# Kernel tuning notes

Measured on AMD Instinct MI355X. Metric: run time of the kernel, lower is better.

The kernel has to match this reference:

```python
import jax, jax.numpy as jnp
import numpy as np

NUM_HEADS = 16
FEAT_DIM = 1024
COORD_DIM = 128
D_FEAT = FEAT_DIM // NUM_HEADS   # 64
D_COORD = COORD_DIM // NUM_HEADS # 8

def setup_inputs() -> dict:
    key = jax.random.key(0)
    ks = jax.random.split(key, 5)
    B, L, S = 2, 2048, 2048
    qf = jax.random.normal(ks[0], (B, L, FEAT_DIM), dtype=jnp.float32)
    kf = jax.random.normal(ks[1], (B, S, FEAT_DIM), dtype=jnp.float32)
    qc = jax.random.normal(ks[2], (B, L, COORD_DIM), dtype=jnp.float32)
    kc = jax.random.normal(ks[3], (B, S, COORD_DIM), dtype=jnp.float32)
    v = jax.random.normal(ks[4], (B, S, FEAT_DIM), dtype=jnp.float32)
    alpha = jnp.ones((NUM_HEADS,), dtype=jnp.float32)
    return {"qf": qf, "kf": kf, "qc": qc, "kc": kc, "v": v, "alpha": alpha}

def _split_heads(x):
    # (B, L, H*D) -> (B, H, L, D)
    B, L, HD = x.shape
    return x.reshape(B, L, NUM_HEADS, HD // NUM_HEADS).transpose(0, 2, 1, 3)

def reference(qf, kf, qc, kc, v, alpha):
    qfh = _split_heads(qf)  # (B,H,L,Df)
    kfh = _split_heads(kf)  # (B,H,S,Df)
    qch = _split_heads(qc)  # (B,H,L,Dc)
    kch = _split_heads(kc)  # (B,H,S,Dc)
    vh = _split_heads(v)    # (B,H,S,Dv)
    # A = softmax(Qf Kf^T / sqrt(Df) + alpha * Qc Kc^T / sqrt(Dc))
    inv_sf = 1.0 / np.sqrt(D_FEAT).astype(np.float32)
    inv_sc = 1.0 / np.sqrt(D_COORD).astype(np.float32)
    scores = (jnp.einsum('bhld,bhsd->bhls', qfh, kfh) * inv_sf
              + alpha[None, :, None, None]
              * jnp.einsum('bhld,bhsd->bhls', qch, kch) * inv_sc)
    attn = jax.nn.softmax(scores, axis=-1)
    out = jnp.einsum('bhls,bhsd->bhld', attn, vh)  # (B,H,L,Dv)
    B, H, L, Dv = out.shape
    return out.transpose(0, 2, 1, 3).reshape(B, L, H * Dv)
```

## Files before the change

### kernel.cpp

```cpp
#include <hip/hip_runtime.h>
#include <hip/hip_bf16.h>

typedef __bf16 bf16_t;
typedef bf16_t bf16x8 __attribute__((ext_vector_type(8)));
typedef float f32x4 __attribute__((ext_vector_type(4)));
typedef float f32x16 __attribute__((ext_vector_type(16)));

#define NHEADS 16
#define DFEAT 64
#define DCOORD 8
#define SEQ 2048
#define KVBLK 64
#define NT (SEQ / KVBLK)
#define QBLK 128
#define KCOLS 80
#define KROWB (KCOLS * 2)
#define KTILEB (KVBLK * KROWB)
#define VSTRB 80
#define VHALFB (DFEAT * VSTRB)
#define VTILEB (2 * VHALFB)

#define KP_BYTES ((size_t)32 * NT * KTILEB)
#define VT_BYTES ((size_t)32 * NT * VTILEB)

union Bf8 { bf16x8 v; __hip_bfloat16 e[8]; };
union U4  { unsigned u[4]; bf16x8 v; };

static __device__ inline unsigned pack2(float a, float b) {
    union { __hip_bfloat16 h[2]; unsigned u; } x;
    x.h[0] = __float2bfloat16(a); x.h[1] = __float2bfloat16(b);
    return x.u;
}

__global__ __launch_bounds__(256)
void pack_kv(const float* __restrict__ kf, const float* __restrict__ kc,
             const float* __restrict__ v,
             char* __restrict__ kp, char* __restrict__ vt)
{
    __shared__ __align__(16) char tile[KTILEB];
    const int bid = blockIdx.x;
    const int tid = threadIdx.x;

    if (bid < 1024) {
        const int blk = bid;
        const int t  = blk & (NT - 1);
        const int bh = blk >> 5;
        const int b = bh >> 4, h = bh & 15;
        #pragma unroll
        for (int it = 0; it < 2; ++it) {
            const int c = tid + it * 256;
            if (c < 320) {
                const int row = c / 5, cc = c - row * 5;
                const int s = t * KVBLK + row;
                float vv[16];
                if (cc < 4) {
                    const float* p = kf + ((long)b * SEQ + s) * (NHEADS * DFEAT) + h * DFEAT + cc * 16;
                    #pragma unroll
                    for (int i = 0; i < 4; ++i) {
                        float4 f = ((const float4*)p)[i];
                        vv[4*i+0]=f.x; vv[4*i+1]=f.y; vv[4*i+2]=f.z; vv[4*i+3]=f.w;
                    }
                } else {
                    const float* p = kc + ((long)b * SEQ + s) * (NHEADS * DCOORD) + h * DCOORD;
                    float4 f0 = ((const float4*)p)[0];
                    float4 f1 = ((const float4*)p)[1];
                    vv[0]=f0.x; vv[1]=f0.y; vv[2]=f0.z; vv[3]=f0.w;
                    vv[4]=f1.x; vv[5]=f1.y; vv[6]=f1.z; vv[7]=f1.w;
                    #pragma unroll
                    for (int i = 8; i < 16; ++i) vv[i] = 0.f;
                }
                Bf8 w0, w1;
                #pragma unroll
                for (int i = 0; i < 8; ++i) {
                    w0.e[i] = __float2bfloat16(vv[i]);
                    w1.e[i] = __float2bfloat16(vv[i + 8]);
                }
                if (cc < 4) {
                    const int key = (row & 7) << 4;
                    const int base = cc * 32;
                    *(bf16x8*)&tile[row * KROWB + ((base)      ^ key)] = w0.v;
                    *(bf16x8*)&tile[row * KROWB + ((base + 16) ^ key)] = w1.v;
                } else {
                    const int key = (row & 1) << 4;
                    *(bf16x8*)&tile[row * KROWB + 128 + ((0)  ^ key)] = w0.v;
                    *(bf16x8*)&tile[row * KROWB + 128 + ((16) ^ key)] = w1.v;
                }
            }
        }
        __syncthreads();
        const bf16x8* ti = (const bf16x8*)tile;
        bf16x8* o = (bf16x8*)(kp + (long)blk * KTILEB);
        #pragma unroll
        for (int j = 0; j < 3; ++j) {
            const int i = tid + 256 * j;
            if (i < 640) o[i] = ti[i];
        }
    } else {
        const int blk = bid - 1024;
        const int t  = blk & (NT - 1);
        const int bh = blk >> 5;
        const int b = bh >> 4, h = bh & 15;
        const int s = tid >> 2, c = tid & 3;
        const int sh = s >> 5, sl = s & 31;
        const int slot = (sl & ~12) | ((sl & 4) << 1) | ((sl & 8) >> 1);
        const float* src = v + ((long)b * SEQ + t * KVBLK + s) * (NHEADS * DFEAT) + h * DFEAT;
        __hip_bfloat16* vtile = (__hip_bfloat16*)tile;
        #pragma unroll
        for (int c4 = 0; c4 < 4; ++c4) {
            float4 f = ((const float4*)src)[c4 * 4 + c];
            float vals[4] = {f.x, f.y, f.z, f.w};
            #pragma unroll
            for (int ii = 0; ii < 4; ++ii) {
                const int dd = c4 * 16 + c * 4 + ii;
                const int byte = sh * VHALFB + dd * VSTRB + slot * 2;
                vtile[byte >> 1] = __float2bfloat16(vals[ii]);
            }
        }
        __syncthreads();
        const bf16x8* ti = (const bf16x8*)tile;
        bf16x8* o = (bf16x8*)(vt + (long)blk * (long)VTILEB);
        #pragma unroll
        for (int j = 0; j < 3; ++j) {
            const int i = tid + 256 * j;
            if (i < 640) o[i] = ti[i];
        }
    }
}

__global__ __launch_bounds__(256, 2)
void stfa_v11(const float* __restrict__ qf, const float* __restrict__ qc,
              const float* __restrict__ alpha,
              const char* __restrict__ kp, const char* __restrict__ vt,
              float* __restrict__ out)
{
    __shared__ __align__(16) char SMEM[2 * KTILEB + 2 * VTILEB];

    const int tid  = threadIdx.x;
    const int wave = tid >> 6;
    const int lane = tid & 63;
    const int lq   = lane & 31;
    const int hi   = lane >> 5;
    const int qp   = wave >> 1;
    const int sh   = wave & 1;

    const int dd    = blockIdx.x;
    const int bh    = dd & 31;
    const int qtile = dd >> 5;
    const int b = bh >> 4, h = bh & 15;

    const float a_h      = alpha[h];
    const float LOG2E    = 1.4426950408889634f;
    const float qf_scale = 0.125f * LOG2E;
    const float qc_scale = a_h * 0.35355339059327373f * LOG2E;

    const char* kp_bh = kp + (long)bh * NT * KTILEB;

    long voff[5];
    #pragma unroll
    for (int j = 0; j < 5; ++j) {
        const int c = wave + 4 * j;
        voff[j] = (c < 10) ? ((long)c * 1024 + lane * 16)
                           : ((long)KP_BYTES + (long)(c - 10) * 1024 + lane * 16);
    }
    int ldsoff[5];
    #pragma unroll
    for (int j = 0; j < 5; ++j) {
        const int c = wave + 4 * j;
        ldsoff[j] = (c < 10) ? c * 1024 : 2 * KTILEB + (c - 10) * 1024;
    }

    auto stage = [&](const char* kg_run, const int BB) {
        #pragma unroll
        for (int j = 0; j < 5; ++j) {
            __builtin_amdgcn_global_load_lds(
                (const __attribute__((address_space(1))) void*)(kg_run + voff[j]),
                (__attribute__((address_space(3))) void*)(SMEM + ldsoff[j] + BB), 16, 0, 0);
        }
    };

    const int krow = sh * 32 + lq;
    int qkaddr[5];
    #pragma unroll
    for (int ks = 0; ks < 5; ++ks) {
        int off;
        if (ks < 4) off = (ks * 32 + hi * 16) ^ ((lq & 7) << 4);
        else        off = 128 + ((hi * 16) ^ ((lq & 1) << 4));
        qkaddr[ks] = krow * KROWB + off;
    }
    int pvaddr[4];
    #pragma unroll
    for (int dt = 0; dt < 2; ++dt)
        #pragma unroll
        for (int ks = 0; ks < 2; ++ks)
            pvaddr[dt * 2 + ks] = sh * VHALFB + (dt * 32 + lq) * VSTRB + ks * 32 + hi * 16;

    const int qrowA = qtile * QBLK + qp * 64 + lq;
    const int qrowB = qrowA + 32;

    bf16x8 qfragA[5], qfragB[5];
    #pragma unroll
    for (int set = 0; set < 2; ++set) {
        const int qrow = set ? qrowB : qrowA;
        const float* qfp = qf + ((long)b * SEQ + qrow) * (NHEADS * DFEAT) + h * DFEAT;
        const float* qcp = qc + ((long)b * SEQ + qrow) * (NHEADS * DCOORD) + h * DCOORD;
        #pragma unroll
        for (int ks = 0; ks < 4; ++ks) {
            const float* p = qfp + ks * 16 + hi * 8;
            float4 f0 = *(const float4*)p;
            float4 f1 = *(const float4*)(p + 4);
            Bf8 q;
        q.e[0] = __float2bfloat16(f0.x * qf_scale); q.e[1] = __float2bfloat16(f0.y * qf_scale);
        q.e[2] = __float2bfloat16(f0.z * qf_scale); q.e[3] = __float2bfloat16(f0.w * qf_scale);
        q.e[4] = __float2bfloat16(f1.x * qf_scale); q.e[5] = __float2bfloat16(f1.y * qf_scale);
        q.e[6] = __float2bfloat16(f1.z * qf_scale); q.e[7] = __float2bfloat16(f1.w * qf_scale);
            if (set) qfragB[ks] = q.v; else qfragA[ks] = q.v;
        }
        Bf8 q;
        #pragma unroll
        for (int i = 0; i < 8; ++i) q.e[i] = __float2bfloat16(0.0f);
        if (hi == 0) {
            float4 c0 = *(const float4*)qcp;
            float4 c1 = *(const float4*)(qcp + 4);
            q.e[0] = __float2bfloat16(c0.x * qc_scale); q.e[1] = __float2bfloat16(c0.y * qc_scale);
            q.e[2] = __float2bfloat16(c0.z * qc_scale); q.e[3] = __float2bfloat16(c0.w * qc_scale);
            q.e[4] = __float2bfloat16(c1.x * qc_scale); q.e[5] = __float2bfloat16(c1.y * qc_scale);
            q.e[6] = __float2bfloat16(c1.z * qc_scale); q.e[7] = __float2bfloat16(c1.w * qc_scale);
        }
        if (set) qfragB[4] = q.v; else qfragA[4] = q.v;
    }

    f32x16 oaccA[2], oaccB[2];
    #pragma unroll
    for (int dt = 0; dt < 2; ++dt)
        #pragma unroll
        for (int r = 0; r < 16; ++r) { oaccA[dt][r] = 0.f; oaccB[dt][r] = 0.f; }
    float lA = 0.f, lB = 0.f;

    auto body = [&](const int KB, const int VB) {
        f32x16 sA, sB;
        #pragma unroll
        for (int r = 0; r < 16; ++r) { sA[r] = 0.f; sB[r] = 0.f; }
        __builtin_amdgcn_s_setprio(1);
        #pragma unroll
        for (int ks = 0; ks < 5; ++ks) {
            bf16x8 kfrag = *(const bf16x8*)&SMEM[KB + qkaddr[ks]];
            sA = __builtin_amdgcn_mfma_f32_32x32x16_bf16(kfrag, qfragA[ks], sA, 0, 0, 0);
            sB = __builtin_amdgcn_mfma_f32_32x32x16_bf16(kfrag, qfragB[ks], sB, 0, 0, 0);
        }
        __builtin_amdgcn_s_setprio(0);

        bf16x8 pA[2], pB[2];
        {
            float p[16];
            #pragma unroll
            for (int r = 0; r < 16; ++r) p[r] = __builtin_amdgcn_exp2f(sA[r]);
            U4 fa, fb;
            #pragma unroll
            for (int i = 0; i < 4; ++i) {
                fa.u[i] = pack2(p[2 * i],     p[2 * i + 1]);
                fb.u[i] = pack2(p[2 * i + 8], p[2 * i + 9]);
            }
            pA[0] = fa.v; pA[1] = fb.v;
            float s8[8];
            #pragma unroll
            for (int r = 0; r < 8; ++r) s8[r] = p[r] + p[r + 8];
            float s4[4];
            #pragma unroll
            for (int r = 0; r < 4; ++r) s4[r] = s8[r] + s8[r + 4];
            lA += (s4[0] + s4[1]) + (s4[2] + s4[3]);
        }
        {
            float p[16];
            #pragma unroll
            for (int r = 0; r < 16; ++r) p[r] = __builtin_amdgcn_exp2f(sB[r]);
            U4 fa, fb;
            #pragma unroll
            for (int i = 0; i < 4; ++i) {
                fa.u[i] = pack2(p[2 * i],     p[2 * i + 1]);
                fb.u[i] = pack2(p[2 * i + 8], p[2 * i + 9]);
            }
            pB[0] = fa.v; pB[1] = fb.v;
            float s8[8];
            #pragma unroll
            for (int r = 0; r < 8; ++r) s8[r] = p[r] + p[r + 8];
            float s4[4];
            #pragma unroll
            for (int r = 0; r < 4; ++r) s4[r] = s8[r] + s8[r + 4];
            lB += (s4[0] + s4[1]) + (s4[2] + s4[3]);
        }

        __builtin_amdgcn_s_setprio(1);
        #pragma unroll
        for (int dt = 0; dt < 2; ++dt) {
            #pragma unroll
            for (int ks = 0; ks < 2; ++ks) {
                bf16x8 vfrag = *(const bf16x8*)&SMEM[VB + pvaddr[dt * 2 + ks]];
                oaccA[dt] = __builtin_amdgcn_mfma_f32_32x32x16_bf16(vfrag, pA[ks], oaccA[dt], 0, 0, 0);
                oaccB[dt] = __builtin_amdgcn_mfma_f32_32x32x16_bf16(vfrag, pB[ks], oaccB[dt], 0, 0, 0);
            }
        }
        __builtin_amdgcn_s_setprio(0);
    };

    const char* kg_run = kp_bh;
    stage(kg_run, 0);
    kg_run += KTILEB;
    __syncthreads();

    for (int t = 0; t < NT; t += 2) {
        stage(kg_run, KTILEB);
        kg_run += KTILEB;
        body(0, 2 * KTILEB);
        __syncthreads();
        if (t + 2 < NT) { stage(kg_run, 0); kg_run += KTILEB; }
        body(KTILEB, 2 * KTILEB + VTILEB);
        __syncthreads();
    }

    float lA2 = lA + __shfl_xor(lA, 32);
    float lB2 = lB + __shfl_xor(lB, 32);

    float* sO = (float*)SMEM;
    float* sL = (float*)(SMEM + 32768);
    if (sh == 1) {
        float* dst = sO + ((qp * 2 + 0) * 64 + lane) * 32;
        #pragma unroll
        for (int dt = 0; dt < 2; ++dt)
            #pragma unroll
            for (int r = 0; r < 16; ++r) dst[dt * 16 + r] = oaccA[dt][r];
        dst = sO + ((qp * 2 + 1) * 64 + lane) * 32;
        #pragma unroll
        for (int dt = 0; dt < 2; ++dt)
            #pragma unroll
            for (int r = 0; r < 16; ++r) dst[dt * 16 + r] = oaccB[dt][r];
        sL[(qp * 2 + 0) * 64 + lane] = lA2;
        sL[(qp * 2 + 1) * 64 + lane] = lB2;
    }
    __syncthreads();
    if (sh == 0) {
        {
            const float* src = sO + ((qp * 2 + 0) * 64 + lane) * 32;
            #pragma unroll
            for (int dt = 0; dt < 2; ++dt)
                #pragma unroll
                for (int r = 0; r < 16; ++r) oaccA[dt][r] += src[dt * 16 + r];
            const float lT = lA2 + sL[(qp * 2 + 0) * 64 + lane];
            const float invl = 1.0f / lT;
            float* ob = out + ((long)b * SEQ + qrowA) * (NHEADS * DFEAT) + h * DFEAT;
            #pragma unroll
            for (int dt = 0; dt < 2; ++dt) {
                #pragma unroll
                for (int g = 0; g < 4; ++g) {
                    const int d0 = dt * 32 + g * 8 + hi * 4;
                    float4 o;
                    o.x = oaccA[dt][4 * g + 0] * invl;
                    o.y = oaccA[dt][4 * g + 1] * invl;
                    o.z = oaccA[dt][4 * g + 2] * invl;
                    o.w = oaccA[dt][4 * g + 3] * invl;
                    *(float4*)(ob + d0) = o;
                }
            }
        }
        {
            const float* src = sO + ((qp * 2 + 1) * 64 + lane) * 32;
            #pragma unroll
            for (int dt = 0; dt < 2; ++dt)
                #pragma unroll
                for (int r = 0; r < 16; ++r) oaccB[dt][r] += src[dt * 16 + r];
            const float lT = lB2 + sL[(qp * 2 + 1) * 64 + lane];
            const float invl = 1.0f / lT;
            float* ob = out + ((long)b * SEQ + qrowB) * (NHEADS * DFEAT) + h * DFEAT;
            #pragma unroll
            for (int dt = 0; dt < 2; ++dt) {
                #pragma unroll
                for (int g = 0; g < 4; ++g) {
                    const int d0 = dt * 32 + g * 8 + hi * 4;
                    float4 o;
                    o.x = oaccB[dt][4 * g + 0] * invl;
                    o.y = oaccB[dt][4 * g + 1] * invl;
                    o.z = oaccB[dt][4 * g + 2] * invl;
                    o.w = oaccB[dt][4 * g + 3] * invl;
                    *(float4*)(ob + d0) = o;
                }
            }
        }
    }
}

__global__ __launch_bounds__(256)
void stfa_v1(const float* __restrict__ qf, const float* __restrict__ kf,
             const float* __restrict__ qc, const float* __restrict__ kc,
             const float* __restrict__ vv, const float* __restrict__ alpha,
             float* __restrict__ out)
{
    __shared__ __align__(16) __hip_bfloat16 Klds[64 * 104];
    __shared__ __align__(16) __hip_bfloat16 Vlds[64 * 72];
    __shared__ __align__(16) __hip_bfloat16 Plds[4 * 16 * 72];

    const int tid  = threadIdx.x;
    const int wave = tid >> 6;
    const int lane = tid & 63;
    const int lr   = lane & 15;
    const int lg   = lane >> 4;

    const int blk   = blockIdx.x;
    const int qtile = blk & 31;
    const int h     = (blk >> 5) & 15;
    const int b     = blk >> 9;

    for (int i = tid; i < 64 * 104; i += 256) Klds[i] = __float2bfloat16(0.0f);

    const float a_h      = alpha[h];
    const float LOG2E    = 1.4426950408889634f;
    const float qf_scale = 0.125f * LOG2E;
    const float qc_scale = a_h * 0.35355339059327373f * LOG2E;

    const int qrow = qtile * 64 + wave * 16 + lr;
    const float* qf_p = qf + ((long)b * SEQ + qrow) * 1024 + h * 64;
    const float* qc_p = qc + ((long)b * SEQ + qrow) * 128 + h * 8;

    bf16x8 qfrag[3];
    #pragma unroll
    for (int st = 0; st < 2; ++st) {
        const float* p = qf_p + st * 32 + lg * 8;
        float4 f0 = *(const float4*)p;
        float4 f1 = *(const float4*)(p + 4);
        Bf8 q;
        q.e[0] = __float2bfloat16(f0.x * qf_scale); q.e[1] = __float2bfloat16(f0.y * qf_scale);
        q.e[2] = __float2bfloat16(f0.z * qf_scale); q.e[3] = __float2bfloat16(f0.w * qf_scale);
        q.e[4] = __float2bfloat16(f1.x * qf_scale); q.e[5] = __float2bfloat16(f1.y * qf_scale);
        q.e[6] = __float2bfloat16(f1.z * qf_scale); q.e[7] = __float2bfloat16(f1.w * qf_scale);
        qfrag[st] = q.v;
    }
    {
        Bf8 q;
        #pragma unroll
        for (int i = 0; i < 8; ++i) q.e[i] = __float2bfloat16(0.0f);
        if (lg == 0) {
            float4 c0 = *(const float4*)qc_p;
            float4 c1 = *(const float4*)(qc_p + 4);
            q.e[0] = __float2bfloat16(c0.x * qc_scale); q.e[1] = __float2bfloat16(c0.y * qc_scale);
            q.e[2] = __float2bfloat16(c0.z * qc_scale); q.e[3] = __float2bfloat16(c0.w * qc_scale);
            q.e[4] = __float2bfloat16(c1.x * qc_scale); q.e[5] = __float2bfloat16(c1.y * qc_scale);
            q.e[6] = __float2bfloat16(c1.z * qc_scale); q.e[7] = __float2bfloat16(c1.w * qc_scale);
        }
        qfrag[2] = q.v;
    }

    const float* kf_b = kf + (long)b * SEQ * 1024 + h * 64;
    const float* kc_b = kc + (long)b * SEQ * 128 + h * 8;
    const float* v_b  = vv + (long)b * SEQ * 1024 + h * 64;

    f32x4 oacc[4];
    #pragma unroll
    for (int ct = 0; ct < 4; ++ct) { oacc[ct][0]=0.f; oacc[ct][1]=0.f; oacc[ct][2]=0.f; oacc[ct][3]=0.f; }
    float m_r[4], l_r[4];
    #pragma unroll
    for (int j = 0; j < 4; ++j) { m_r[j] = -3.0e38f; l_r[j] = 0.f; }

    __syncthreads();

    for (int s0 = 0; s0 < SEQ; s0 += 64) {
        {
            const int srow = tid >> 2, ch = tid & 3;
            const float* p = kf_b + (long)(s0 + srow) * 1024 + ch * 16;
            float4 f0 = ((const float4*)p)[0];
            float4 f1 = ((const float4*)p)[1];
            float4 f2 = ((const float4*)p)[2];
            float4 f3 = ((const float4*)p)[3];
            Bf8 w0, w1;
            w0.e[0]=__float2bfloat16(f0.x); w0.e[1]=__float2bfloat16(f0.y);
            w0.e[2]=__float2bfloat16(f0.z); w0.e[3]=__float2bfloat16(f0.w);
            w0.e[4]=__float2bfloat16(f1.x); w0.e[5]=__float2bfloat16(f1.y);
            w0.e[6]=__float2bfloat16(f1.z); w0.e[7]=__float2bfloat16(f1.w);
            w1.e[0]=__float2bfloat16(f2.x); w1.e[1]=__float2bfloat16(f2.y);
            w1.e[2]=__float2bfloat16(f2.z); w1.e[3]=__float2bfloat16(f2.w);
            w1.e[4]=__float2bfloat16(f3.x); w1.e[5]=__float2bfloat16(f3.y);
            w1.e[6]=__float2bfloat16(f3.z); w1.e[7]=__float2bfloat16(f3.w);
            *(bf16x8*)&Klds[srow * 104 + ch * 16]     = w0.v;
            *(bf16x8*)&Klds[srow * 104 + ch * 16 + 8] = w1.v;
        }
        {
            const int srow = tid >> 2, cp = (tid & 3) * 2;
            const float* p = kc_b + (long)(s0 + srow) * 128 + cp;
            float2 c = *(const float2*)p;
            Klds[srow * 104 + 64 + cp]     = __float2bfloat16(c.x);
            Klds[srow * 104 + 64 + cp + 1] = __float2bfloat16(c.y);
        }
        {
            const int srow = tid & 63, d0 = (tid >> 6) * 16;
            const float* p = v_b + (long)(s0 + srow) * 1024 + d0;
            #pragma unroll
            for (int c4 = 0; c4 < 4; ++c4) {
                float4 f = ((const float4*)p)[c4];
                Vlds[(d0 + c4 * 4 + 0) * 72 + srow] = __float2bfloat16(f.x);
                Vlds[(d0 + c4 * 4 + 1) * 72 + srow] = __float2bfloat16(f.y);
                Vlds[(d0 + c4 * 4 + 2) * 72 + srow] = __float2bfloat16(f.z);
                Vlds[(d0 + c4 * 4 + 3) * 72 + srow] = __float2bfloat16(f.w);
            }
        }
        __syncthreads();

        f32x4 sacc[4];
        #pragma unroll
        for (int ct = 0; ct < 4; ++ct) { sacc[ct][0]=0.f; sacc[ct][1]=0.f; sacc[ct][2]=0.f; sacc[ct][3]=0.f; }
        #pragma unroll
        for (int ct = 0; ct < 4; ++ct) {
            #pragma unroll
            for (int st = 0; st < 3; ++st) {
                bf16x8 kfrag = *(const bf16x8*)&Klds[(ct * 16 + lr) * 104 + st * 32 + lg * 8];
                sacc[ct] = __builtin_amdgcn_mfma_f32_16x16x32_bf16(qfrag[st], kfrag, sacc[ct], 0, 0, 0);
            }
        }

        float rs[4];
        #pragma unroll
        for (int j = 0; j < 4; ++j) {
            float mx = fmaxf(fmaxf(sacc[0][j], sacc[1][j]), fmaxf(sacc[2][j], sacc[3][j]));
            mx = fmaxf(mx, __shfl_xor(mx, 1));
            mx = fmaxf(mx, __shfl_xor(mx, 2));
            mx = fmaxf(mx, __shfl_xor(mx, 4));
            mx = fmaxf(mx, __shfl_xor(mx, 8));
            float nm = fmaxf(m_r[j], mx);
            rs[j] = __builtin_amdgcn_exp2f(m_r[j] - nm);
            m_r[j] = nm;
        }
        __hip_bfloat16* myP = Plds + wave * 16 * 72;
        #pragma unroll
        for (int j = 0; j < 4; ++j) {
            float p0 = __builtin_amdgcn_exp2f(sacc[0][j] - m_r[j]);
            float p1 = __builtin_amdgcn_exp2f(sacc[1][j] - m_r[j]);
            float p2 = __builtin_amdgcn_exp2f(sacc[2][j] - m_r[j]);
            float p3 = __builtin_amdgcn_exp2f(sacc[3][j] - m_r[j]);
            const int r = lg * 4 + j;
            myP[r * 72 +  0 + lr] = __float2bfloat16(p0);
            myP[r * 72 + 16 + lr] = __float2bfloat16(p1);
            myP[r * 72 + 32 + lr] = __float2bfloat16(p2);
            myP[r * 72 + 48 + lr] = __float2bfloat16(p3);
            float sum = p0 + p1 + p2 + p3;
            sum += __shfl_xor(sum, 1);
            sum += __shfl_xor(sum, 2);
            sum += __shfl_xor(sum, 4);
            sum += __shfl_xor(sum, 8);
            l_r[j] = l_r[j] * rs[j] + sum;
            oacc[0][j] *= rs[j]; oacc[1][j] *= rs[j];
            oacc[2][j] *= rs[j]; oacc[3][j] *= rs[j];
        }

        #pragma unroll
        for (int kk = 0; kk < 2; ++kk) {
            bf16x8 pfrag = *(const bf16x8*)&myP[lr * 72 + kk * 32 + lg * 8];
            #pragma unroll
            for (int ct = 0; ct < 4; ++ct) {
                bf16x8 vfrag = *(const bf16x8*)&Vlds[(ct * 16 + lr) * 72 + kk * 32 + lg * 8];
                oacc[ct] = __builtin_amdgcn_mfma_f32_16x16x32_bf16(pfrag, vfrag, oacc[ct], 0, 0, 0);
            }
        }
        __syncthreads();
    }

    #pragma unroll
    for (int j = 0; j < 4; ++j) {
        const float invl = 1.0f / l_r[j];
        const int q = qtile * 64 + wave * 16 + lg * 4 + j;
        float* op = out + ((long)b * SEQ + q) * 1024 + h * 64;
        op[ 0 + lr] = oacc[0][j] * invl;
        op[16 + lr] = oacc[1][j] * invl;
        op[32 + lr] = oacc[2][j] * invl;
        op[48 + lr] = oacc[3][j] * invl;
    }
}

extern "C" void kernel_launch(void* const* d_in, const int* in_sizes, int n_in,
                              void* d_out, int out_size, void* d_ws, size_t ws_size,
                              hipStream_t stream) {
    const float* qf    = (const float*)d_in[0];
    const float* kf    = (const float*)d_in[1];
    const float* qc    = (const float*)d_in[2];
    const float* kc    = (const float*)d_in[3];
    const float* vv    = (const float*)d_in[4];
    const float* alpha = (const float*)d_in[5];
    float* out = (float*)d_out;

    const int B = 2;
    if (ws_size >= KP_BYTES + VT_BYTES) {
        char* kp = (char*)d_ws;
        char* vt = (char*)d_ws + KP_BYTES;
        pack_kv<<<2 * B * NHEADS * NT, 256, 0, stream>>>(kf, kc, vv, kp, vt);
        stfa_v11<<<B * NHEADS * (SEQ / QBLK), 256, 0, stream>>>(qf, qc, alpha, kp, vt, out);
    } else {
        stfa_v1<<<B * NHEADS * (SEQ / 64), 256, 0, stream>>>(qf, kf, qc, kc, vv, alpha, out);
    }
}
```

Baseline: 65.28 us.

## Double KV tile to 128 rows, halving loop iterations and barriers

Raises the KV block from 64 to 128 keys. Each wave now computes two 32-key score sub-tiles per step and runs four PV k-steps, and the pack kernel and the V tile layout (stride 144) are reworked to match. Staging now loads K and V separately using per-wave offsets. The aim is to halve the number of barriers and pipeline stages and to give more MFMA work between syncs. The cost is roughly double the LDS footprint and more registers, which could hurt occupancy at 2 blocks per CU.

```diff
diff --git a/kernel.cpp b/kernel.cpp
--- a/kernel.cpp
+++ b/kernel.cpp
@@ -10,18 +10,23 @@
 #define DFEAT 64
 #define DCOORD 8
 #define SEQ 2048
-#define KVBLK 64
+#define KVBLK 128
 #define NT (SEQ / KVBLK)
 #define QBLK 128
 #define KCOLS 80
 #define KROWB (KCOLS * 2)
 #define KTILEB (KVBLK * KROWB)
-#define VSTRB 80
+#define VSTRB 144
 #define VHALFB (DFEAT * VSTRB)
 #define VTILEB (2 * VHALFB)
 
 #define KP_BYTES ((size_t)32 * NT * KTILEB)
 #define VT_BYTES ((size_t)32 * NT * VTILEB)
+
+#define K1_OFF  KTILEB
+#define V0_OFF  (2 * KTILEB)
+#define V1_OFF  (2 * KTILEB + VTILEB)
+#define SMEM_SZ (2 * KTILEB + 2 * VTILEB)
 
 union Bf8 { bf16x8 v; __hip_bfloat16 e[8]; };
 union U4  { unsigned u[4]; bf16x8 v; };
@@ -41,15 +46,15 @@
     const int bid = blockIdx.x;
     const int tid = threadIdx.x;
 
-    if (bid < 1024) {
+    if (bid < 512) {
         const int blk = bid;
         const int t  = blk & (NT - 1);
-        const int bh = blk >> 5;
+        const int bh = blk >> 4;
         const int b = bh >> 4, h = bh & 15;
         #pragma unroll
-        for (int it = 0; it < 2; ++it) {
+        for (int it = 0; it < 3; ++it) {
             const int c = tid + it * 256;
-            if (c < 320) {
+            if (c < 640) {
                 const int row = c / 5, cc = c - row * 5;
                 const int s = t * KVBLK + row;
                 float vv[16];
@@ -91,49 +96,50 @@
         const bf16x8* ti = (const bf16x8*)tile;
         bf16x8* o = (bf16x8*)(kp + (long)blk * KTILEB);
         #pragma unroll
-        for (int j = 0; j < 3; ++j) {
-            const int i = tid + 256 * j;
-            if (i < 640) o[i] = ti[i];
-        }
+        for (int j = 0; j < 5; ++j) o[tid + 256 * j] = ti[tid + 256 * j];
     } else {
-        const int blk = bid - 1024;
+        const int blk = bid - 512;
         const int t  = blk & (NT - 1);
-        const int bh = blk >> 5;
+        const int bh = blk >> 4;
         const int b = bh >> 4, h = bh & 15;
-        const int s = tid >> 2, c = tid & 3;
-        const int sh = s >> 5, sl = s & 31;
-        const int slot = (sl & ~12) | ((sl & 4) << 1) | ((sl & 8) >> 1);
-        const float* src = v + ((long)b * SEQ + t * KVBLK + s) * (NHEADS * DFEAT) + h * DFEAT;
         __hip_bfloat16* vtile = (__hip_bfloat16*)tile;
         #pragma unroll
-        for (int c4 = 0; c4 < 4; ++c4) {
-            float4 f = ((const float4*)src)[c4 * 4 + c];
-            float vals[4] = {f.x, f.y, f.z, f.w};
-            #pragma unroll
-            for (int ii = 0; ii < 4; ++ii) {
-                const int dd = c4 * 16 + c * 4 + ii;
-                const int byte = sh * VHALFB + dd * VSTRB + slot * 2;
-                vtile[byte >> 1] = __float2bfloat16(vals[ii]);
+        for (int it = 0; it < 2; ++it) {
+            const int s = (tid >> 2) + it * 64;
+            const int c = tid & 3;
+            const int shh = s >> 6, sl = s & 63;
+            const int stile = sl >> 5, sl32 = sl & 31;
+            const int slot = (sl32 & ~12) | ((sl32 & 4) << 1) | ((sl32 & 8) >> 1);
+            const float* src = v + ((long)b * SEQ + t * KVBLK + s) * (NHEADS * DFEAT) + h * DFEAT;
+            #pragma unroll
+            for (int c4 = 0; c4 < 4; ++c4) {
+                float4 f = ((const float4*)src)[c4 * 4 + c];
+                float vals[4] = {f.x, f.y, f.z, f.w};
+                #pragma unroll
+                for (int ii = 0; ii < 4; ++ii) {
+                    const int d8 = c4 * 16 + c * 4 + ii;
+                    vtile[shh * 4608 + d8 * 72 + stile * 32 + slot] = __float2bfloat16(vals[ii]);
+                }
             }
         }
         __syncthreads();
         const bf16x8* ti = (const bf16x8*)tile;
         bf16x8* o = (bf16x8*)(vt + (long)blk * (long)VTILEB);
         #pragma unroll
-        for (int j = 0; j < 3; ++j) {
+        for (int j = 0; j < 5; ++j) {
             const int i = tid + 256 * j;
-            if (i < 640) o[i] = ti[i];
+            if (i < 1152) o[i] = ti[i];
         }
     }
 }
 
 __global__ __launch_bounds__(256, 2)
-void stfa_v11(const float* __restrict__ qf, const float* __restrict__ qc,
+void stfa_v12(const float* __restrict__ qf, const float* __restrict__ qc,
               const float* __restrict__ alpha,
               const char* __restrict__ kp, const char* __restrict__ vt,
               float* __restrict__ out)
 {
-    __shared__ __align__(16) char SMEM[2 * KTILEB + 2 * VTILEB];
+    __shared__ __align__(16) char SMEM[SMEM_SZ];
 
     const int tid  = threadIdx.x;
     const int wave = tid >> 6;
@@ -154,45 +160,52 @@
     const float qc_scale = a_h * 0.35355339059327373f * LOG2E;
 
     const char* kp_bh = kp + (long)bh * NT * KTILEB;
-
-    long voff[5];
+    const char* vt_bh = vt + (long)bh * NT * VTILEB;
+
+    long kvoff[5], vvoff[5];
+    int  kloff[5], vloff[5];
     #pragma unroll
     for (int j = 0; j < 5; ++j) {
-        const int c = wave + 4 * j;
-        voff[j] = (c < 10) ? ((long)c * 1024 + lane * 16)
-                           : ((long)KP_BYTES + (long)(c - 10) * 1024 + lane * 16);
-    }
-    int ldsoff[5];
-    #pragma unroll
-    for (int j = 0; j < 5; ++j) {
-        const int c = wave + 4 * j;
-        ldsoff[j] = (c < 10) ? c * 1024 : 2 * KTILEB + (c - 10) * 1024;
-    }
-
-    auto stage = [&](const char* kg_run, const int BB) {
-        #pragma unroll
-        for (int j = 0; j < 5; ++j) {
+        const int kc_ = wave + 4 * j;
+        kvoff[j] = (long)kc_ * 1024 + lane * 16;
+        kloff[j] = kc_ * 1024;
+        vvoff[j] = (long)kc_ * 1024 + lane * 16;
+        vloff[j] = V0_OFF + kc_ * 1024;
+    }
+    const int nV = (wave + 16 < 18) ? 5 : 4;
+
+    auto stage = [&](const char* kt, const char* vtp, const int KOFF, const int VOFF) {
+        #pragma unroll
+        for (int j = 0; j < 5; ++j)
             __builtin_amdgcn_global_load_lds(
-                (const __attribute__((address_space(1))) void*)(kg_run + voff[j]),
-                (__attribute__((address_space(3))) void*)(SMEM + ldsoff[j] + BB), 16, 0, 0);
-        }
+                (const __attribute__((address_space(1))) void*)(kt + kvoff[j]),
+                (__attribute__((address_space(3))) void*)(SMEM + kloff[j] + KOFF), 16, 0, 0);
+        #pragma unroll
+        for (int j = 0; j < 5; ++j)
+            if (j < nV)
+                __builtin_amdgcn_global_load_lds(
+                    (const __attribute__((address_space(1))) void*)(vtp + vvoff[j]),
+                    (__attribute__((address_space(3))) void*)(SMEM + vloff[j] + VOFF), 16, 0, 0);
     };
 
-    const int krow = sh * 32 + lq;
-    int qkaddr[5];
-    #pragma unroll
-    for (int ks = 0; ks < 5; ++ks) {
-        int off;
-        if (ks < 4) off = (ks * 32 + hi * 16) ^ ((lq & 7) << 4);
-        else        off = 128 + ((hi * 16) ^ ((lq & 1) << 4));
-        qkaddr[ks] = krow * KROWB + off;
-    }
-    int pvaddr[4];
+    int qkaddr[2][5];
+    #pragma unroll
+    for (int st = 0; st < 2; ++st) {
+        const int krow = sh * 64 + st * 32 + lq;
+        #pragma unroll
+        for (int ks = 0; ks < 5; ++ks) {
+            int off;
+            if (ks < 4) off = (ks * 32 + hi * 16) ^ ((lq & 7) << 4);
+            else        off = 128 + ((hi * 16) ^ ((lq & 1) << 4));
+            qkaddr[st][ks] = krow * KROWB + off;
+        }
+    }
+    int pvaddr[2][4];
     #pragma unroll
     for (int dt = 0; dt < 2; ++dt)
         #pragma unroll
-        for (int ks = 0; ks < 2; ++ks)
-            pvaddr[dt * 2 + ks] = sh * VHALFB + (dt * 32 + lq) * VSTRB + ks * 32 + hi * 16;
+        for (int ks = 0; ks < 4; ++ks)
+            pvaddr[dt][ks] = sh * VHALFB + (dt * 32 + lq) * VSTRB + ks * 32 + hi * 16;
 
     const int qrowA = qtile * QBLK + qp * 64 + lq;
     const int qrowB = qrowA + 32;
@@ -209,10 +222,10 @@
             float4 f0 = *(const float4*)p;
             float4 f1 = *(const float4*)(p + 4);
             Bf8 q;
-        q.e[0] = __float2bfloat16(f0.x * qf_scale); q.e[1] = __float2bfloat16(f0.y * qf_scale);
-        q.e[2] = __float2bfloat16(f0.z * qf_scale); q.e[3] = __float2bfloat16(f0.w * qf_scale);
-        q.e[4] = __float2bfloat16(f1.x * qf_scale); q.e[5] = __float2bfloat16(f1.y * qf_scale);
-        q.e[6] = __float2bfloat16(f1.z * qf_scale); q.e[7] = __float2bfloat16(f1.w * qf_scale);
+            q.e[0] = __float2bfloat16(f0.x * qf_scale); q.e[1] = __float2bfloat16(f0.y * qf_scale);
+            q.e[2] = __float2bfloat16(f0.z * qf_scale); q.e[3] = __float2bfloat16(f0.w * qf_scale);
+            q.e[4] = __float2bfloat16(f1.x * qf_scale); q.e[5] = __float2bfloat16(f1.y * qf_scale);
+            q.e[6] = __float2bfloat16(f1.z * qf_scale); q.e[7] = __float2bfloat16(f1.w * qf_scale);
             if (set) qfragB[ks] = q.v; else qfragA[ks] = q.v;
         }
         Bf8 q;
@@ -236,65 +249,54 @@
         for (int r = 0; r < 16; ++r) { oaccA[dt][r] = 0.f; oaccB[dt][r] = 0.f; }
     float lA = 0.f, lB = 0.f;
 
+    auto do_sm = [&](const f32x16& S, bf16x8& f0o, bf16x8& f1o, float& lacc) {
+        float p[16];
+        #pragma unroll
+        for (int r = 0; r < 16; ++r) p[r] = __builtin_amdgcn_exp2f(S[r]);
+        U4 fa, fb;
+        #pragma unroll
+        for (int i = 0; i < 4; ++i) {
+            fa.u[i] = pack2(p[2 * i],     p[2 * i + 1]);
+            fb.u[i] = pack2(p[2 * i + 8], p[2 * i + 9]);
+        }
+        f0o = fa.v; f1o = fb.v;
+        float s8[8];
+        #pragma unroll
+        for (int r = 0; r < 8; ++r) s8[r] = p[r] + p[r + 8];
+        float s4[4];
+        #pragma unroll
+        for (int r = 0; r < 4; ++r) s4[r] = s8[r] + s8[r + 4];
+        lacc += (s4[0] + s4[1]) + (s4[2] + s4[3]);
+    };
+
     auto body = [&](const int KB, const int VB) {
-        f32x16 sA, sB;
-        #pragma unroll
-        for (int r = 0; r < 16; ++r) { sA[r] = 0.f; sB[r] = 0.f; }
+        f32x16 s0A, s0B, s1A, s1B;
+        #pragma unroll
+        for (int r = 0; r < 16; ++r) { s0A[r]=0.f; s0B[r]=0.f; s1A[r]=0.f; s1B[r]=0.f; }
         __builtin_amdgcn_s_setprio(1);
         #pragma unroll
         for (int ks = 0; ks < 5; ++ks) {
-            bf16x8 kfrag = *(const bf16x8*)&SMEM[KB + qkaddr[ks]];
-            sA = __builtin_amdgcn_mfma_f32_32x32x16_bf16(kfrag, qfragA[ks], sA, 0, 0, 0);
-            sB = __builtin_amdgcn_mfma_f32_32x32x16_bf16(kfrag, qfragB[ks], sB, 0, 0, 0);
+            bf16x8 k0 = *(const bf16x8*)&SMEM[KB + qkaddr[0][ks]];
+            bf16x8 k1 = *(const bf16x8*)&SMEM[KB + qkaddr[1][ks]];
+            s0A = __builtin_amdgcn_mfma_f32_32x32x16_bf16(k0, qfragA[ks], s0A, 0, 0, 0);
+            s0B = __builtin_amdgcn_mfma_f32_32x32x16_bf16(k0, qfragB[ks], s0B, 0, 0, 0);
+            s1A = __builtin_amdgcn_mfma_f32_32x32x16_bf16(k1, qfragA[ks], s1A, 0, 0, 0);
+            s1B = __builtin_amdgcn_mfma_f32_32x32x16_bf16(k1, qfragB[ks], s1B, 0, 0, 0);
         }
         __builtin_amdgcn_s_setprio(0);
 
-        bf16x8 pA[2], pB[2];
-        {
-            float p[16];
-            #pragma unroll
-            for (int r = 0; r < 16; ++r) p[r] = __builtin_amdgcn_exp2f(sA[r]);
-            U4 fa, fb;
-            #pragma unroll
-            for (int i = 0; i < 4; ++i) {
-                fa.u[i] = pack2(p[2 * i],     p[2 * i + 1]);
-                fb.u[i] = pack2(p[2 * i + 8], p[2 * i + 9]);
-            }
-            pA[0] = fa.v; pA[1] = fb.v;
-            float s8[8];
-            #pragma unroll
-            for (int r = 0; r < 8; ++r) s8[r] = p[r] + p[r + 8];
-            float s4[4];
-            #pragma unroll
-            for (int r = 0; r < 4; ++r) s4[r] = s8[r] + s8[r + 4];
-            lA += (s4[0] + s4[1]) + (s4[2] + s4[3]);
-        }
-        {
-            float p[16];
-            #pragma unroll
-            for (int r = 0; r < 16; ++r) p[r] = __builtin_amdgcn_exp2f(sB[r]);
-            U4 fa, fb;
-            #pragma unroll
-            for (int i = 0; i < 4; ++i) {
-                fa.u[i] = pack2(p[2 * i],     p[2 * i + 1]);
-                fb.u[i] = pack2(p[2 * i + 8], p[2 * i + 9]);
-            }
-            pB[0] = fa.v; pB[1] = fb.v;
-            float s8[8];
-            #pragma unroll
-            for (int r = 0; r < 8; ++r) s8[r] = p[r] + p[r + 8];
-            float s4[4];
-            #pragma unroll
-            for (int r = 0; r < 4; ++r) s4[r] = s8[r] + s8[r + 4];
-            lB += (s4[0] + s4[1]) + (s4[2] + s4[3]);
-        }
+        bf16x8 pA[4], pB[4];
+        do_sm(s0A, pA[0], pA[1], lA);
+        do_sm(s0B, pB[0], pB[1], lB);
+        do_sm(s1A, pA[2], pA[3], lA);
+        do_sm(s1B, pB[2], pB[3], lB);
 
         __builtin_amdgcn_s_setprio(1);
         #pragma unroll
         for (int dt = 0; dt < 2; ++dt) {
             #pragma unroll
-            for (int ks = 0; ks < 2; ++ks) {
-                bf16x8 vfrag = *(const bf16x8*)&SMEM[VB + pvaddr[dt * 2 + ks]];
+            for (int ks = 0; ks < 4; ++ks) {
+                bf16x8 vfrag = *(const bf16x8*)&SMEM[VB + pvaddr[dt][ks]];
                 oaccA[dt] = __builtin_amdgcn_mfma_f32_32x32x16_bf16(vfrag, pA[ks], oaccA[dt], 0, 0, 0);
                 oaccB[dt] = __builtin_amdgcn_mfma_f32_32x32x16_bf16(vfrag, pB[ks], oaccB[dt], 0, 0, 0);
             }
@@ -302,18 +304,18 @@
         __builtin_amdgcn_s_setprio(0);
     };
 
-    const char* kg_run = kp_bh;
-    stage(kg_run, 0);
-    kg_run += KTILEB;
+    stage(kp_bh, vt_bh, 0, 0);
     __syncthreads();
 
+    const char* kt  = kp_bh + KTILEB;
+    const char* vtp = vt_bh + VTILEB;
+
     for (int t = 0; t < NT; t += 2) {
-        stage(kg_run, KTILEB);
-        kg_run += KTILEB;
-        body(0, 2 * KTILEB);
+        stage(kt, vtp, K1_OFF, VTILEB); kt += KTILEB; vtp += VTILEB;
+        body(0, V0_OFF);
         __syncthreads();
-        if (t + 2 < NT) { stage(kg_run, 0); kg_run += KTILEB; }
-        body(KTILEB, 2 * KTILEB + VTILEB);
+        if (t + 2 < NT) { stage(kt, vtp, 0, 0); kt += KTILEB; vtp += VTILEB; }
+        body(K1_OFF, V1_OFF);
         __syncthreads();
     }
 
@@ -586,8 +588,8 @@
     if (ws_size >= KP_BYTES + VT_BYTES) {
         char* kp = (char*)d_ws;
         char* vt = (char*)d_ws + KP_BYTES;
-        pack_kv<<<2 * B * NHEADS * NT, 256, 0, stream>>>(kf, kc, vv, kp, vt);
-        stfa_v11<<<B * NHEADS * (SEQ / QBLK), 256, 0, stream>>>(qf, qc, alpha, kp, vt, out);
+        pack_kv<<<1024, 256, 0, stream>>>(kf, kc, vv, kp, vt);
+        stfa_v12<<<B * NHEADS * (SEQ / QBLK), 256, 0, stream>>>(qf, qc, alpha, kp, vt, out);
     } else {
         stfa_v1<<<B * NHEADS * (SEQ / 64), 256, 0, stream>>>(qf, kf, qc, kc, vv, alpha, out);
     }
```

After: 66.27 us. Within noise of the previous version (+1.5%).
